# Optimization experiments

Hardware: AMD Instinct MI355X
Metric: run time of the kernel (lower is better)

Reference implementation:

```python
import jax, jax.numpy as jnp
import numpy as np

NB, HD, NL, NF = 5, 64, 4, 10           # num_bins, hidden_dim(d_model), num_layers, num_frames
DI, DS, DC, DTR = 128, 16, 4, 4          # d_inner=2*HD, d_state, d_conv, dt_rank=ceil(HD/16)
B, H, W = 4, 64, 64


def _conv2d(x, w, b):
    y = jax.lax.conv_general_dilated(x, w, (1, 1), 'SAME',
                                     dimension_numbers=('NCHW', 'OIHW', 'NCHW'))
    return y + b[None, :, None, None]


def _bn_relu(x, gamma, beta, eps=1e-5):
    # BatchNorm2d in training mode: biased batch stats over (N,H,W)
    mean = x.mean(axis=(0, 2, 3), keepdims=True)
    var = x.var(axis=(0, 2, 3), keepdims=True)
    y = (x - mean) * jax.lax.rsqrt(var + eps)
    return jax.nn.relu(y * gamma[None, :, None, None] + beta[None, :, None, None])


def _silu(x):
    return x * jax.nn.sigmoid(x)


def _causal_dwconv(x, w, b):
    # x: (B,L,DI), w: (DI,K) depthwise causal conv, b: (DI,)
    K = w.shape[1]
    L = x.shape[1]
    xp = jnp.pad(x, ((0, 0), (K - 1, 0), (0, 0)))
    y = sum(xp[:, k:k + L, :] * w[:, k] for k in range(K))
    return y + b


def _selective_scan(u, delta, A, Bm, Cm, D):
    # u,delta: (B,L,DI); A: (DI,DS); Bm,Cm: (B,L,DS); D: (DI,)
    dT, BT, CT, uT = (t.transpose(1, 0, 2) for t in (delta, Bm, Cm, u))
    h0 = jnp.zeros((u.shape[0], A.shape[0], A.shape[1]), u.dtype)

    def step(h, inp):
        d_t, B_t, C_t, u_t = inp                     # (B,DI),(B,DS),(B,DS),(B,DI)
        dA = jnp.exp(d_t[:, :, None] * A)            # (B,DI,DS)
        h = dA * h + (d_t * u_t)[:, :, None] * B_t[:, None, :]
        y = jnp.einsum('bds,bs->bd', h, C_t)
        return h, y

    _, ys = jax.lax.scan(step, h0, (dT, BT, CT, uT))  # ys: (L,B,DI)
    return ys.transpose(1, 0, 2) + u * D


def _mamba(x, in_proj, conv_w, conv_b, x_proj, dt_w, dt_b, A_log, Dp, out_proj):
    xz = x @ in_proj.T                               # (B,L,2*DI)
    xi, z = jnp.split(xz, 2, axis=-1)
    xi = _silu(_causal_dwconv(xi, conv_w, conv_b))
    xdbc = xi @ x_proj.T                             # (B,L,DTR+2*DS)
    dt, Bm, Cm = jnp.split(xdbc, [DTR, DTR + DS], axis=-1)
    delta = jax.nn.softplus(dt @ dt_w.T + dt_b)
    A = -jnp.exp(A_log)
    y = _selective_scan(xi, delta, A, Bm, Cm, Dp)
    return (y * _silu(z)) @ out_proj.T


def setup_inputs() -> dict:
    key = jax.random.key(0)
    ks = jax.random.split(key, 20)
    s = 0.02
    inp = {
        'x': jax.random.normal(ks[0], (B, NB, H, W), jnp.float32),
        'enc_w': jax.random.normal(ks[1], (HD, NB, 3, 3), jnp.float32) * s,
        'enc_b': jnp.zeros((HD,), jnp.float32),
        'enc_g': jnp.ones((HD,), jnp.float32),
        'enc_be': jnp.zeros((HD,), jnp.float32),
        'in_proj': jax.random.normal(ks[2], (NL, 2 * DI, HD), jnp.float32) * s,
        'conv_w': jax.random.normal(ks[3], (NL, DI, DC), jnp.float32) * s,
        'conv_b': jnp.zeros((NL, DI), jnp.float32),
        'x_proj': jax.random.normal(ks[4], (NL, DTR + 2 * DS, DI), jnp.float32) * s,
        'dt_w': jax.random.normal(ks[5], (NL, DI, DTR), jnp.float32) * s,
        'dt_b': jax.random.normal(ks[6], (NL, DI), jnp.float32) * 0.1 - 4.0,
        'A_log': jnp.broadcast_to(jnp.log(jnp.arange(1, DS + 1, dtype=jnp.float32)),
                                  (NL, DI, DS)).copy(),
        'Dp': jnp.ones((NL, DI), jnp.float32),
        'out_proj': jax.random.normal(ks[7], (NL, HD, DI), jnp.float32) * s,
        'dec1_w': jax.random.normal(ks[8], (HD, HD, 3, 3), jnp.float32) * s,
        'dec1_b': jnp.zeros((HD,), jnp.float32),
        'dec1_g': jnp.ones((HD,), jnp.float32),
        'dec1_be': jnp.zeros((HD,), jnp.float32),
        'dec2_w': jax.random.normal(ks[9], (NF, HD, 3, 3), jnp.float32) * s,
        'dec2_b': jnp.zeros((NF,), jnp.float32),
    }
    return inp


def reference(x, enc_w, enc_b, enc_g, enc_be, in_proj, conv_w, conv_b, x_proj,
              dt_w, dt_b, A_log, Dp, out_proj, dec1_w, dec1_b, dec1_g, dec1_be,
              dec2_w, dec2_b):
    Bb, _, Hh, Ww = x.shape
    h = _bn_relu(_conv2d(x, enc_w, enc_b), enc_g, enc_be)   # (B,HD,H,W)
    t = h.reshape(Bb, HD, Hh * Ww).transpose(0, 2, 1)        # (B,L,HD)
    for i in range(NL):
        t = t + _mamba(t, in_proj[i], conv_w[i], conv_b[i], x_proj[i],
                       dt_w[i], dt_b[i], A_log[i], Dp[i], out_proj[i])
    h = t.transpose(0, 2, 1).reshape(Bb, HD, Hh, Ww)
    h = _bn_relu(_conv2d(h, dec1_w, dec1_b), dec1_g, dec1_be)
    return _conv2d(h, dec2_w, dec2_b)                        # (B,NF,H,W)
```

## Files before the change

kernel.cpp:

```cpp
#include <hip/hip_runtime.h>
#include <hip/hip_bf16.h>

#define BB   4
#define NBC  5
#define HD   64
#define NLAYER 4
#define NFC  10
#define DIM  128
#define DSN  16
#define DCN  4
#define DTRK 4
#define HH   64
#define WWD  64
#define LL   4096
#define MM   (BB*LL)
#define NCHUNK 128
#define CLEN   32
#define TSTEP  16

__global__ void k_prep_all(const float* __restrict__ in_proj, const float* __restrict__ out_proj,
                           const float* __restrict__ dec1_w, const float* __restrict__ dec2_w,
                           float* __restrict__ wTin, float* __restrict__ wTout,
                           float* __restrict__ wT1, float* __restrict__ wT2,
                           float* __restrict__ stats, float* __restrict__ stats2) {
    int idx = blockIdx.x * blockDim.x + threadIdx.x;
    if (idx < 65536) {
        int n = idx & 255, k = (idx >> 8) & 63, l = idx >> 14;
        wTin[idx] = in_proj[(l << 14) + (n << 6) + k];
    } else if (idx < 98304) {
        int j = idx - 65536;
        int n = j & 63, k = (j >> 6) & 127, l = j >> 13;
        wTout[j] = out_proj[(l << 13) + (n << 7) + k];
    } else if (idx < 135168) {
        int j = idx - 98304;
        int co = j & 63, tap = (j >> 6) % 9, ci = j / 576;
        wT1[j] = dec1_w[co * 576 + ci * 9 + tap];
    } else if (idx < 142848) {
        int j = idx - 135168;
        int tap = j % 12, t2 = j / 12, co = t2 % NFC, ci = t2 / NFC;
        wT2[j] = (tap < 9) ? dec2_w[co * 576 + ci * 9 + tap] : 0.f;
    } else if (idx < 143104) {
        int j = idx - 142848;
        if (j < 128) stats[j] = 0.f; else stats2[j - 128] = 0.f;
    }
}

__global__ void k_enc_conv(const float* __restrict__ x, const float* __restrict__ w,
                           const float* __restrict__ bias, float* __restrict__ out,
                           float* __restrict__ stats) {
    __shared__ float r1[256], r2[256];
    int tid = threadIdx.x;
    int idx = blockIdx.x * 256 + tid;
    int wx = idx & 63;
    int hy = (idx >> 6) & 63;
    int co = (idx >> 12) & 63;
    int b  = idx >> 18;
    float acc = bias[co];
    for (int ci = 0; ci < NBC; ++ci) {
        const float* xin = x + (((long)(b * NBC + ci)) << 12);
        const float* wp  = w + (co * NBC + ci) * 9;
        #pragma unroll
        for (int kh = 0; kh < 3; ++kh) {
            int ih = hy + kh - 1;
            if (ih < 0 || ih >= HH) continue;
            #pragma unroll
            for (int kw = 0; kw < 3; ++kw) {
                int iw = wx + kw - 1;
                if (iw < 0 || iw >= WWD) continue;
                acc += xin[(ih << 6) + iw] * wp[kh * 3 + kw];
            }
        }
    }
    out[idx] = acc;
    r1[tid] = acc; r2[tid] = acc * acc;
    __syncthreads();
    for (int off = 128; off > 0; off >>= 1) {
        if (tid < off) { r1[tid] += r1[tid + off]; r2[tid] += r2[tid + off]; }
        __syncthreads();
    }
    if (tid == 0) {
        atomicAdd(&stats[co], r1[0]);
        atomicAdd(&stats[64 + co], r2[0]);
    }
}

__global__ void k_bn_tr_seq(const float* __restrict__ src, const float* __restrict__ stats,
                            const float* __restrict__ g, const float* __restrict__ be,
                            float* __restrict__ tout) {
    __shared__ float s[64 * 65];
    __shared__ float sc[64], sh[64];
    int blk = blockIdx.x;
    int b = blk >> 6;
    int hw0 = (blk & 63) << 6;
    int tid = threadIdx.x;
    if (tid < 64) {
        float m = stats[tid] * (1.f / 16384.f);
        float var = stats[64 + tid] * (1.f / 16384.f) - m * m;
        float ss = g[tid] * rsqrtf(var + 1e-5f);
        sc[tid] = ss; sh[tid] = be[tid] - m * ss;
    }
    for (int i = tid; i < 4096; i += 256) {
        int pix = i & 63, c = i >> 6;
        s[c * 65 + pix] = src[((long)((b << 6) + c) << 12) + hw0 + pix];
    }
    __syncthreads();
    for (int i = tid; i < 4096; i += 256) {
        int c = i & 63, pix = i >> 6;
        float y = s[c * 65 + pix] * sc[c] + sh[c];
        tout[((long)((b << 12) + hw0 + pix) << 6) + c] = fmaxf(y, 0.f);
    }
}

__global__ __launch_bounds__(256, 1) void k_gemm_in2(const float* __restrict__ tin,
                                                     const float* __restrict__ wT,
                                                     float* __restrict__ xz) {
    __shared__ __align__(16) float ts[64 * 68];
    long m0 = (long)blockIdx.x << 6;
    int tid = threadIdx.x;
    int rg = tid >> 5;
    int cg = tid & 31;
    for (int i = tid; i < 4096; i += 256) {
        int r = i >> 6, k = i & 63;
        ts[r * 68 + k] = tin[(m0 << 6) + i];
    }
    __syncthreads();
    float acc[8][8] = {};
    int n0 = cg << 3;
    for (int k4 = 0; k4 < 16; ++k4) {
        float4 a[8];
        #pragma unroll
        for (int r2 = 0; r2 < 8; ++r2)
            a[r2] = *(const float4*)&ts[((rg << 3) + r2) * 68 + (k4 << 2)];
        #pragma unroll
        for (int kk = 0; kk < 4; ++kk) {
            const float* wr = wT + (((k4 << 2) + kk) << 8) + n0;
            float4 w0 = *(const float4*)&wr[0];
            float4 w1 = *(const float4*)&wr[4];
            #pragma unroll
            for (int r2 = 0; r2 < 8; ++r2) {
                float av = (kk == 0) ? a[r2].x : (kk == 1) ? a[r2].y
                         : (kk == 2) ? a[r2].z : a[r2].w;
                acc[r2][0] += av * w0.x; acc[r2][1] += av * w0.y;
                acc[r2][2] += av * w0.z; acc[r2][3] += av * w0.w;
                acc[r2][4] += av * w1.x; acc[r2][5] += av * w1.y;
                acc[r2][6] += av * w1.z; acc[r2][7] += av * w1.w;
            }
        }
    }
    #pragma unroll
    for (int r2 = 0; r2 < 8; ++r2) {
        long m = m0 + (rg << 3) + r2;
        *(float4*)&xz[(m << 8) + n0]     = make_float4(acc[r2][0], acc[r2][1], acc[r2][2], acc[r2][3]);
        *(float4*)&xz[(m << 8) + n0 + 4] = make_float4(acc[r2][4], acc[r2][5], acc[r2][6], acc[r2][7]);
    }
}

__global__ __launch_bounds__(256, 1) void k_gemm_oi(const float* __restrict__ gated,
                                                    const float* __restrict__ wTo,
                                                    const float* __restrict__ wTi,
                                                    float* __restrict__ tio,
                                                    float* __restrict__ xz) {
    __shared__ __align__(16) float g_s[64 * 132];
    __shared__ __align__(16) float t_s[64 * 68];
    long m0 = (long)blockIdx.x << 6;
    int tid = threadIdx.x;
    for (int i = tid; i < 8192; i += 256) {
        int r = i >> 7, k = i & 127;
        g_s[r * 132 + k] = gated[(m0 << 7) + i];
    }
    __syncthreads();
    {
        int rg = tid >> 4, cg = tid & 15;
        int n0 = cg << 2;
        float acc[4][4] = {};
        for (int k4 = 0; k4 < 32; ++k4) {
            float4 a[4];
            #pragma unroll
            for (int r2 = 0; r2 < 4; ++r2)
                a[r2] = *(const float4*)&g_s[((rg << 2) + r2) * 132 + (k4 << 2)];
            #pragma unroll
            for (int kk = 0; kk < 4; ++kk) {
                const float* wr = wTo + (((k4 << 2) + kk) << 6) + n0;
                float4 w0 = *(const float4*)&wr[0];
                #pragma unroll
                for (int r2 = 0; r2 < 4; ++r2) {
                    float av = (kk == 0) ? a[r2].x : (kk == 1) ? a[r2].y
                             : (kk == 2) ? a[r2].z : a[r2].w;
                    acc[r2][0] += av * w0.x; acc[r2][1] += av * w0.y;
                    acc[r2][2] += av * w0.z; acc[r2][3] += av * w0.w;
                }
            }
        }
        #pragma unroll
        for (int r2 = 0; r2 < 4; ++r2) {
            long m = m0 + (rg << 2) + r2;
            float4 t0 = *(const float4*)&tio[(m << 6) + n0];
            t0.x += acc[r2][0]; t0.y += acc[r2][1];
            t0.z += acc[r2][2]; t0.w += acc[r2][3];
            *(float4*)&tio[(m << 6) + n0] = t0;
            *(float4*)&t_s[((rg << 2) + r2) * 68 + n0] = t0;
        }
    }
    __syncthreads();
    {
        int rg = tid >> 5, cg = tid & 31;
        int n0 = cg << 3;
        float acc[8][8] = {};
        for (int k4 = 0; k4 < 16; ++k4) {
            float4 a[8];
            #pragma unroll
            for (int r2 = 0; r2 < 8; ++r2)
                a[r2] = *(const float4*)&t_s[((rg << 3) + r2) * 68 + (k4 << 2)];
            #pragma unroll
            for (int kk = 0; kk < 4; ++kk) {
                const float* wr = wTi + (((k4 << 2) + kk) << 8) + n0;
                float4 w0 = *(const float4*)&wr[0];
                float4 w1 = *(const float4*)&wr[4];
                #pragma unroll
                for (int r2 = 0; r2 < 8; ++r2) {
                    float av = (kk == 0) ? a[r2].x : (kk == 1) ? a[r2].y
                             : (kk == 2) ? a[r2].z : a[r2].w;
                    acc[r2][0] += av * w0.x; acc[r2][1] += av * w0.y;
                    acc[r2][2] += av * w0.z; acc[r2][3] += av * w0.w;
                    acc[r2][4] += av * w1.x; acc[r2][5] += av * w1.y;
                    acc[r2][6] += av * w1.z; acc[r2][7] += av * w1.w;
                }
            }
        }
        #pragma unroll
        for (int r2 = 0; r2 < 8; ++r2) {
            long m = m0 + (rg << 3) + r2;
            *(float4*)&xz[(m << 8) + n0]     = make_float4(acc[r2][0], acc[r2][1], acc[r2][2], acc[r2][3]);
            *(float4*)&xz[(m << 8) + n0 + 4] = make_float4(acc[r2][4], acc[r2][5], acc[r2][6], acc[r2][7]);
        }
    }
}

__global__ __launch_bounds__(256, 1) void k_gemm_out2(const float* __restrict__ gated,
                                                      const float* __restrict__ wT,
                                                      float* __restrict__ tio) {
    __shared__ __align__(16) float ts[64 * 132];
    long m0 = (long)blockIdx.x << 6;
    int tid = threadIdx.x;
    int rg = tid >> 4;
    int cg = tid & 15;
    for (int i = tid; i < 8192; i += 256) {
        int r2 = i >> 7, k = i & 127;
        ts[r2 * 132 + k] = gated[(m0 << 7) + i];
    }
    __syncthreads();
    float acc[4][4] = {};
    int n0 = cg << 2;
    for (int k4 = 0; k4 < 32; ++k4) {
        float4 a[4];
        #pragma unroll
        for (int r2 = 0; r2 < 4; ++r2)
            a[r2] = *(const float4*)&ts[((rg << 2) + r2) * 132 + (k4 << 2)];
        #pragma unroll
        for (int kk = 0; kk < 4; ++kk) {
            const float* wr = wT + (((k4 << 2) + kk) << 6) + n0;
            float4 w0 = *(const float4*)&wr[0];
            #pragma unroll
            for (int r2 = 0; r2 < 4; ++r2) {
                float av = (kk == 0) ? a[r2].x : (kk == 1) ? a[r2].y
                         : (kk == 2) ? a[r2].z : a[r2].w;
                acc[r2][0] += av * w0.x; acc[r2][1] += av * w0.y;
                acc[r2][2] += av * w0.z; acc[r2][3] += av * w0.w;
            }
        }
    }
    #pragma unroll
    for (int r2 = 0; r2 < 4; ++r2) {
        long m = m0 + (rg << 2) + r2;
        float4 t0 = *(const float4*)&tio[(m << 6) + n0];
        t0.x += acc[r2][0]; t0.y += acc[r2][1];
        t0.z += acc[r2][2]; t0.w += acc[r2][3];
        *(float4*)&tio[(m << 6) + n0] = t0;
    }
}

__global__ void k_xproj_fused(const float* __restrict__ xz, const float* __restrict__ cw,
                              const float* __restrict__ cb, const float* __restrict__ Wx,
                              const float* __restrict__ dw, const float* __restrict__ dbias,
                              float* __restrict__ xi, float* __restrict__ xdbc,
                              float* __restrict__ delta) {
    __shared__ float xz_s[35 * 132];
    __shared__ float xi_s[32 * 132];
    __shared__ float w_s[36 * 132];
    __shared__ float xs[32 * 40];
    __shared__ float cwT[4 * 128];
    __shared__ float cb_s[128];
    long m0 = (long)blockIdx.x << 5;
    int l0 = (int)(m0 & 4095);
    int tid = threadIdx.x;

    for (int i = tid; i < 35 * 128; i += 256) {
        int j = i >> 7, k = i & 127;
        int l = l0 - 3 + j;
        float v = 0.f;
        if (l >= 0) v = xz[(m0 - 3 + j) * 256 + k];
        xz_s[j * 132 + k] = v;
    }
    if (tid < 128) cb_s[tid] = cb[tid];
    for (int i = tid; i < 512; i += 256) {
        int kk = i >> 7, di = i & 127;
        cwT[(kk << 7) + di] = cw[(di << 2) + kk];
    }
    for (int i = tid; i < 4608; i += 256) {
        int n = i >> 7, k = i & 127;
        w_s[n * 132 + k] = Wx[i];
    }
    __syncthreads();

    for (int ii = 0; ii < 4; ++ii) {
        int i = tid + (ii << 8);
        int r = i >> 5;
        int d4 = (i & 31) << 2;
        float4 a = *(const float4*)&cb_s[d4];
        #pragma unroll
        for (int kk = 0; kk < 4; ++kk) {
            float4 xv = *(const float4*)&xz_s[(r + kk) * 132 + d4];
            float4 wv = *(const float4*)&cwT[(kk << 7) + d4];
            a.x += xv.x * wv.x; a.y += xv.y * wv.y;
            a.z += xv.z * wv.z; a.w += xv.w * wv.w;
        }
        a.x = a.x / (1.f + __expf(-a.x));
        a.y = a.y / (1.f + __expf(-a.y));
        a.z = a.z / (1.f + __expf(-a.z));
        a.w = a.w / (1.f + __expf(-a.w));
        *(float4*)&xi_s[r * 132 + d4] = a;
        *(float4*)&xi[(m0 + r) * 128 + d4] = a;
    }
    __syncthreads();

    int n = tid & 63;
    int rg = tid >> 6;
    if (n < 36) {
        float acc[8] = {0,0,0,0,0,0,0,0};
        for (int k4 = 0; k4 < 32; ++k4) {
            float4 w4 = *(const float4*)&w_s[n * 132 + (k4 << 2)];
            #pragma unroll
            for (int r = 0; r < 8; ++r) {
                float4 a4 = *(const float4*)&xi_s[((rg << 3) + r) * 132 + (k4 << 2)];
                acc[r] += a4.x * w4.x + a4.y * w4.y + a4.z * w4.z + a4.w * w4.w;
            }
        }
        #pragma unroll
        for (int r = 0; r < 8; ++r) {
            int rr = (rg << 3) + r;
            xdbc[(m0 + rr) * 36 + n] = acc[r];
            xs[rr * 40 + n] = acc[r];
        }
    }
    __syncthreads();
    for (int i = tid; i < 4096; i += 256) {
        int r = i >> 7, di = i & 127;
        float v = dbias[di];
        float4 d4 = *(const float4*)&dw[di << 2];
        v += xs[r * 40 + 0] * d4.x + xs[r * 40 + 1] * d4.y
           + xs[r * 40 + 2] * d4.z + xs[r * 40 + 3] * d4.w;
        delta[(m0 + r) * 128 + di] = (v > 20.f) ? v : log1pf(expf(v));
    }
}

__global__ void k_scan_p1(const float* __restrict__ delta, const float* __restrict__ xi,
                          const float* __restrict__ xdbc, const float* __restrict__ A_log,
                          float* __restrict__ Pb, float* __restrict__ Sb) {
    __shared__ float d_s[TSTEP][64];
    __shared__ float u_s[TSTEP][64];
    __shared__ float b_s[TSTEP][16];
    int chunk = blockIdx.x, b = blockIdx.y, half = blockIdx.z;
    int tid = threadIdx.x;
    int dq = tid & 3;
    int dil = tid >> 2;
    int di = (half << 6) + dil;
    float4 al = *(const float4*)&A_log[(di << 4) + (dq << 2)];
    float Av[4] = { -expf(al.x), -expf(al.y), -expf(al.z), -expf(al.w) };
    float h[4] = {0.f, 0.f, 0.f, 0.f};
    float P[4] = {1.f, 1.f, 1.f, 1.f};
    long t0 = ((long)b << 12) + (long)chunk * CLEN;

    int srow = tid >> 4, sc4 = (tid & 15) << 2;
    for (int tile = 0; tile < CLEN / TSTEP; ++tile) {
        __syncthreads();
        long ls = t0 + tile * TSTEP + srow;
        *(float4*)&d_s[srow][sc4] = *(const float4*)&delta[(ls << 7) + (half << 6) + sc4];
        *(float4*)&u_s[srow][sc4] = *(const float4*)&xi[(ls << 7) + (half << 6) + sc4];
        if (tid < 64) {
            int r2 = tid >> 2, cc = (tid & 3) << 2;
            long l2 = t0 + tile * TSTEP + r2;
            *(float4*)&b_s[r2][cc] = *(const float4*)&xdbc[l2 * 36 + DTRK + cc];
        }
        __syncthreads();
        #pragma unroll
        for (int i = 0; i < TSTEP; ++i) {
            float d = d_s[i][dil];
            float u = u_s[i][dil];
            float du = d * u;
            float4 Bv = *(float4*)&b_s[i][dq << 2];
            float a0 = __expf(d * Av[0]); h[0] = a0 * h[0] + du * Bv.x; P[0] *= a0;
            float a1 = __expf(d * Av[1]); h[1] = a1 * h[1] + du * Bv.y; P[1] *= a1;
            float a2 = __expf(d * Av[2]); h[2] = a2 * h[2] + du * Bv.z; P[2] *= a2;
            float a3 = __expf(d * Av[3]); h[3] = a3 * h[3] + du * Bv.w; P[3] *= a3;
        }
    }
    long o = (((long)chunk * BB + b) << 11) + (di << 4) + (dq << 2);
    *(float4*)&Pb[o] = make_float4(P[0], P[1], P[2], P[3]);
    *(float4*)&Sb[o] = make_float4(h[0], h[1], h[2], h[3]);
}

__global__ void k_scan_p2(float* Pb, const float* __restrict__ Sb) {
    int t = blockIdx.x * blockDim.x + threadIdx.x;
    int b = t >> 11;
    int s = t & 2047;
    float h = 0.f;
    for (int c = 0; c < NCHUNK; ++c) {
        long idx = (((long)c * BB + b) << 11) + s;
        float p = Pb[idx];
        float sv = Sb[idx];
        Pb[idx] = h;
        h = p * h + sv;
    }
}

__global__ void k_scan_p3(const float* __restrict__ delta, const float* __restrict__ xi,
                          const float* __restrict__ xdbc, const float* __restrict__ A_log,
                          const float* __restrict__ Dp, const float* __restrict__ xz,
                          const float* __restrict__ hin, float* __restrict__ gated) {
    __shared__ float d_s[TSTEP][64];
    __shared__ float u_s[TSTEP][64];
    __shared__ float bc_s[TSTEP][32];
    __shared__ float y_s[TSTEP][64];
    int chunk = blockIdx.x, b = blockIdx.y, half = blockIdx.z;
    int tid = threadIdx.x;
    int dq = tid & 3;
    int dil = tid >> 2;
    int di = (half << 6) + dil;
    float4 al = *(const float4*)&A_log[(di << 4) + (dq << 2)];
    float Av[4] = { -expf(al.x), -expf(al.y), -expf(al.z), -expf(al.w) };
    float Dv = Dp[di];
    long ho = (((long)chunk * BB + b) << 11) + (di << 4) + (dq << 2);
    float4 h4 = *(const float4*)&hin[ho];
    float h[4] = { h4.x, h4.y, h4.z, h4.w };
    long t0 = ((long)b << 12) + (long)chunk * CLEN;

    int srow = tid >> 4, sc4 = (tid & 15) << 2;
    for (int tile = 0; tile < CLEN / TSTEP; ++tile) {
        __syncthreads();
        long ls = t0 + tile * TSTEP + srow;
        *(float4*)&d_s[srow][sc4] = *(const float4*)&delta[(ls << 7) + (half << 6) + sc4];
        *(float4*)&u_s[srow][sc4] = *(const float4*)&xi[(ls << 7) + (half << 6) + sc4];
        if (tid < 128) {
            int r2 = tid >> 3, cc = (tid & 7) << 2;
            long l2 = t0 + tile * TSTEP + r2;
            *(float4*)&bc_s[r2][cc] = *(const float4*)&xdbc[l2 * 36 + DTRK + cc];
        }
        __syncthreads();
        #pragma unroll
        for (int i = 0; i < TSTEP; ++i) {
            float d = d_s[i][dil];
            float u = u_s[i][dil];
            float du = d * u;
            float4 Bv = *(float4*)&bc_s[i][dq << 2];
            float4 Cv = *(float4*)&bc_s[i][16 + (dq << 2)];
            float a0 = __expf(d * Av[0]); h[0] = a0 * h[0] + du * Bv.x;
            float a1 = __expf(d * Av[1]); h[1] = a1 * h[1] + du * Bv.y;
            float a2 = __expf(d * Av[2]); h[2] = a2 * h[2] + du * Bv.z;
            float a3 = __expf(d * Av[3]); h[3] = a3 * h[3] + du * Bv.w;
            float yp = h[0] * Cv.x + h[1] * Cv.y + h[2] * Cv.z + h[3] * Cv.w;
            yp += __shfl_xor(yp, 1);
            yp += __shfl_xor(yp, 2);
            if (dq == 0)
                y_s[i][dil] = yp + u * Dv;
        }
        __syncthreads();
        {
            long l = t0 + tile * TSTEP + srow;
            float4 y4 = *(float4*)&y_s[srow][sc4];
            float4 z4 = *(const float4*)&xz[(l << 8) + DIM + (half << 6) + sc4];
            float4 og;
            og.x = y4.x * (z4.x / (1.f + __expf(-z4.x)));
            og.y = y4.y * (z4.y / (1.f + __expf(-z4.y)));
            og.z = y4.z * (z4.z / (1.f + __expf(-z4.z)));
            og.w = y4.w * (z4.w / (1.f + __expf(-z4.w)));
            *(float4*)&gated[(l << 7) + (half << 6) + sc4] = og;
        }
    }
}

__global__ __launch_bounds__(256, 1) void k_dec1_new(const float* __restrict__ tin,
                                                     const float* __restrict__ wT,
                                                     const float* __restrict__ bias,
                                                     float* __restrict__ out,
                                                     float* __restrict__ stats2) {
    __shared__ __align__(16) float x_s[64 * 132];
    __shared__ __align__(16) float w_s[4 * 4608];
    int tile = blockIdx.x;
    int b = blockIdx.y;
    int ty0 = (tile >> 3) << 3;
    int tx0 = (tile & 7) << 3;
    int tid = threadIdx.x;
    int wv = tid >> 6;
    int lane = tid & 63;
    int r = lane >> 3;
    int cg = lane & 7;

    for (int i = tid; i < 6400; i += 256) {
        int pl = i >> 6;
        int c = i & 63;
        int py = pl / 10, px = pl - py * 10;
        int ih = ty0 + py - 1, iw = tx0 + px - 1;
        float v = 0.f;
        if (ih >= 0 && ih < HH && iw >= 0 && iw < WWD)
            v = tin[(((long)((b << 12) + (ih << 6) + iw)) << 6) + c];
        x_s[c * 132 + py * 12 + px] = v;
    }
    float* myw = &w_s[wv * 4608];
    const float* gw = wT + (wv * 16) * 576;
    float4 pref[18];
    #pragma unroll
    for (int i = 0; i < 18; ++i)
        pref[i] = *(const float4*)&gw[(i * 64 + lane) * 4];
    #pragma unroll
    for (int i = 0; i < 18; ++i)
        *(float4*)&myw[(i * 64 + lane) * 4] = pref[i];
    __syncthreads();

    float acc[8][8] = {};
    #pragma unroll
    for (int ch = 0; ch < 2; ++ch) {
        if (ch == 0) {
            const float* gw1 = wT + (wv * 16 + 8) * 576;
            #pragma unroll
            for (int i = 0; i < 18; ++i)
                pref[i] = *(const float4*)&gw1[(i * 64 + lane) * 4];
        }
        for (int cl = 0; cl < 8; ++cl) {
            int cib = wv * 16 + ch * 8 + cl;
            float xrow[3][10];
            #pragma unroll
            for (int kh = 0; kh < 3; ++kh) {
                const float* xr = &x_s[cib * 132 + (r + kh) * 12];
                float4 a0 = *(const float4*)&xr[0];
                float4 a1 = *(const float4*)&xr[4];
                float2 a2 = *(const float2*)&xr[8];
                xrow[kh][0] = a0.x; xrow[kh][1] = a0.y; xrow[kh][2] = a0.z; xrow[kh][3] = a0.w;
                xrow[kh][4] = a1.x; xrow[kh][5] = a1.y; xrow[kh][6] = a1.z; xrow[kh][7] = a1.w;
                xrow[kh][8] = a2.x; xrow[kh][9] = a2.y;
            }
            const float* wp = &myw[cl * 576];
            #pragma unroll
            for (int kh = 0; kh < 3; ++kh) {
                #pragma unroll
                for (int kw = 0; kw < 3; ++kw) {
                    const float* wp2 = wp + (kh * 3 + kw) * 64 + (cg << 3);
                    float4 wa = *(const float4*)&wp2[0];
                    float4 wb = *(const float4*)&wp2[4];
                    #pragma unroll
                    for (int j = 0; j < 8; ++j) {
                        float xv = xrow[kh][kw + j];
                        acc[j][0] += xv * wa.x; acc[j][1] += xv * wa.y;
                        acc[j][2] += xv * wa.z; acc[j][3] += xv * wa.w;
                        acc[j][4] += xv * wb.x; acc[j][5] += xv * wb.y;
                        acc[j][6] += xv * wb.z; acc[j][7] += xv * wb.w;
                    }
                }
            }
        }
        if (ch == 0) {
            #pragma unroll
            for (int i = 0; i < 18; ++i)
                *(float4*)&myw[(i * 64 + lane) * 4] = pref[i];
        }
    }

    #pragma unroll
    for (int j = 0; j < 8; ++j) {
        *(float4*)&myw[lane * 68 + (j << 3)]     = make_float4(acc[j][0], acc[j][1], acc[j][2], acc[j][3]);
        *(float4*)&myw[lane * 68 + (j << 3) + 4] = make_float4(acc[j][4], acc[j][5], acc[j][6], acc[j][7]);
    }
    __syncthreads();

    float bv = bias[lane];
    float ssum = 0.f, ssq = 0.f;
    #pragma unroll
    for (int pp = 0; pp < 16; ++pp) {
        int pr = (wv << 1) + (pp >> 3);
        int pc = pp & 7;
        int ol = (pr << 3) + (lane >> 3);
        int ix = (pc << 3) + (lane & 7);
        float s = w_s[ol * 68 + ix] + w_s[4608 + ol * 68 + ix]
                + w_s[9216 + ol * 68 + ix] + w_s[13824 + ol * 68 + ix] + bv;
        out[(((long)((b << 12) + ((ty0 + pr) << 6) + tx0 + pc)) << 6) + lane] = s;
        ssum += s; ssq += s * s;
    }
    float* red = x_s;
    red[(wv << 6) + lane] = ssum;
    red[256 + (wv << 6) + lane] = ssq;
    __syncthreads();
    if (tid < 64) {
        float a = red[tid] + red[64 + tid] + red[128 + tid] + red[192 + tid];
        float q = red[256 + tid] + red[320 + tid] + red[384 + tid] + red[448 + tid];
        atomicAdd(&stats2[tid], a);
        atomicAdd(&stats2[64 + tid], q);
    }
}

__global__ void k_dec2_fused(const float* __restrict__ src, const float* __restrict__ stats2,
                             const float* __restrict__ g, const float* __restrict__ be,
                             const float* __restrict__ wT, const float* __restrict__ bias,
                             float* __restrict__ out) {
    __shared__ float x_s[64 * 101];
    __shared__ float w_s[64 * NFC * 12];
    __shared__ float sc_s[64];
    __shared__ float sh_s[64];
    int tile = blockIdx.x;
    int b = blockIdx.y;
    int ty0 = (tile >> 3) << 3;
    int tx0 = (tile & 7) << 3;
    int tid = threadIdx.x;

    if (tid < 64) {
        float m = stats2[tid] * (1.f / 16384.f);
        float var = stats2[64 + tid] * (1.f / 16384.f) - m * m;
        float s = g[tid] * rsqrtf(var + 1e-5f);
        sc_s[tid] = s;
        sh_s[tid] = be[tid] - m * s;
    }
    for (int i = tid; i < 64 * NFC * 12; i += 256)
        w_s[i] = wT[i];
    __syncthreads();

    for (int i = tid; i < 6400; i += 256) {
        int pl = i >> 6;
        int c = i & 63;
        int py = pl / 10, px = pl - py * 10;
        int ih = ty0 + py - 1, iw = tx0 + px - 1;
        float v = 0.f;
        if (ih >= 0 && ih < HH && iw >= 0 && iw < WWD) {
            v = src[((long)((b << 12) + (ih << 6) + iw)) * 64 + c];
            v = fmaxf(v * sc_s[c] + sh_s[c], 0.f);
        }
        x_s[c * 101 + pl] = v;
    }
    __syncthreads();

    int px = tid & 63;
    int py = px >> 3, pxx = px & 7;
    int cog = tid >> 6;
    float acc[3] = {0.f, 0.f, 0.f};
    int nco = (cog < 2) ? 3 : 2;

    for (int ci = 0; ci < 64; ++ci) {
        const float* xr = &x_s[ci * 101 + py * 10 + pxx];
        float xv[9];
        #pragma unroll
        for (int kh = 0; kh < 3; ++kh)
            #pragma unroll
            for (int kw = 0; kw < 3; ++kw)
                xv[kh * 3 + kw] = xr[kh * 10 + kw];
        #pragma unroll
        for (int j = 0; j < 3; ++j) {
            if (j >= nco) break;
            int co = cog + (j << 2);
            const float* wp = &w_s[(ci * NFC + co) * 12];
            float4 w0 = *(const float4*)&wp[0];
            float4 w1 = *(const float4*)&wp[4];
            float  w8 = wp[8];
            acc[j] += xv[0] * w0.x + xv[1] * w0.y + xv[2] * w0.z + xv[3] * w0.w
                    + xv[4] * w1.x + xv[5] * w1.y + xv[6] * w1.z + xv[7] * w1.w
                    + xv[8] * w8;
        }
    }
    int hw = ((ty0 + py) << 6) + tx0 + pxx;
    #pragma unroll
    for (int j = 0; j < 3; ++j) {
        if (j >= nco) break;
        int co = cog + (j << 2);
        out[((long)(b * NFC + co) << 12) + hw] = acc[j] + bias[co];
    }
}

extern "C" void kernel_launch(void* const* d_in, const int* in_sizes, int n_in,
                              void* d_out, int out_size, void* d_ws, size_t ws_size,
                              hipStream_t stream) {
    const float* x       = (const float*)d_in[0];
    const float* enc_w   = (const float*)d_in[1];
    const float* enc_b   = (const float*)d_in[2];
    const float* enc_g   = (const float*)d_in[3];
    const float* enc_be  = (const float*)d_in[4];
    const float* in_proj = (const float*)d_in[5];
    const float* conv_w  = (const float*)d_in[6];
    const float* conv_b  = (const float*)d_in[7];
    const float* x_proj  = (const float*)d_in[8];
    const float* dt_w    = (const float*)d_in[9];
    const float* dt_b    = (const float*)d_in[10];
    const float* A_log   = (const float*)d_in[11];
    const float* Dp      = (const float*)d_in[12];
    const float* out_prj = (const float*)d_in[13];
    const float* dec1_w  = (const float*)d_in[14];
    const float* dec1_b  = (const float*)d_in[15];
    const float* dec1_g  = (const float*)d_in[16];
    const float* dec1_be = (const float*)d_in[17];
    const float* dec2_w  = (const float*)d_in[18];
    const float* dec2_b  = (const float*)d_in[19];
    float* out = (float*)d_out;

    float* ws = (float*)d_ws;
    size_t off = 0;
    float* conv_buf  = ws + off; off += 1048576;
    float* stats     = ws + off; off += 128;
    float* stats2    = ws + off; off += 128;
    float* wT1       = ws + off; off += 36864;
    float* wT2       = ws + off; off += 7680;
    float* wTin      = ws + off; off += 65536;
    float* wTout     = ws + off; off += 32768;
    float* t_buf     = ws + off; off += 1048576;
    float* xz_buf    = ws + off; off += 4194304;
    float* xi_buf    = ws + off; off += 2097152;
    float* xdbc_buf  = ws + off; off += 589824;
    float* delta_buf = ws + off; off += 2097152;
    float* gated_buf = ws + off; off += 2097152;
    (void)ws_size; (void)in_sizes; (void)n_in; (void)out_size;

    float* Pb = conv_buf;
    float* Sb = gated_buf;

    k_prep_all<<<560, 256, 0, stream>>>(in_proj, out_prj, dec1_w, dec2_w,
                                        wTin, wTout, wT1, wT2, stats, stats2);

    k_enc_conv<<<4096, 256, 0, stream>>>(x, enc_w, enc_b, conv_buf, stats);
    k_bn_tr_seq<<<256, 256, 0, stream>>>(conv_buf, stats, enc_g, enc_be, t_buf);

    dim3 sg(NCHUNK, BB, 2);
    k_gemm_in2<<<256, 256, 0, stream>>>(t_buf, wTin, xz_buf);
    for (int i = 0; i < NLAYER; ++i) {
        k_xproj_fused<<<512, 256, 0, stream>>>(xz_buf, conv_w + i * DIM * DCN,
                                               conv_b + i * DIM, x_proj + i * 36 * DIM,
                                               dt_w + i * DIM * DTRK, dt_b + i * DIM,
                                               xi_buf, xdbc_buf, delta_buf);
        k_scan_p1<<<sg, 256, 0, stream>>>(delta_buf, xi_buf, xdbc_buf,
                                          A_log + i * DIM * DSN, Pb, Sb);
        k_scan_p2<<<32, 256, 0, stream>>>(Pb, Sb);
        k_scan_p3<<<sg, 256, 0, stream>>>(delta_buf, xi_buf, xdbc_buf,
                                          A_log + i * DIM * DSN, Dp + i * DIM,
                                          xz_buf, Pb, gated_buf);
        if (i < NLAYER - 1)
            k_gemm_oi<<<256, 256, 0, stream>>>(gated_buf, wTout + i * 8192,
                                               wTin + (i + 1) * 16384, t_buf, xz_buf);
    }
    k_gemm_out2<<<256, 256, 0, stream>>>(gated_buf, wTout + 3 * 8192, t_buf);

    dim3 dg1(64, BB);
    k_dec1_new<<<dg1, 256, 0, stream>>>(t_buf, wT1, dec1_b, conv_buf, stats2);
    k_dec2_fused<<<dg1, 256, 0, stream>>>(conv_buf, stats2, dec1_g, dec1_be, wT2, dec2_b, out);
}
```

Before: 532.4 us.

## Fuse chunked scan pass 1 into xproj kernel using shared-memory delta and B

The first chunk-scan pass (per-chunk decay product and local state) now runs at the end of the xproj kernel. It uses delta, xi and B values that are already in shared memory, so the separate k_scan_p1 launch and its global re-reads of delta, xi and xdbc go away. Each thread now handles 8 states for one channel, and a launch bound of 256 threads with 2 blocks is added. The risks are higher register pressure and fewer blocks doing the sequential 32-step loop, which could lengthen this kernel's tail.

```diff
diff --git a/kernel.cpp b/kernel.cpp
--- a/kernel.cpp
+++ b/kernel.cpp
@@ -279,11 +279,13 @@
     }
 }
 
-__global__ void k_xproj_fused(const float* __restrict__ xz, const float* __restrict__ cw,
-                              const float* __restrict__ cb, const float* __restrict__ Wx,
-                              const float* __restrict__ dw, const float* __restrict__ dbias,
-                              float* __restrict__ xi, float* __restrict__ xdbc,
-                              float* __restrict__ delta) {
+__global__ __launch_bounds__(256, 2) void k_xproj_fused(
+        const float* __restrict__ xz, const float* __restrict__ cw,
+        const float* __restrict__ cb, const float* __restrict__ Wx,
+        const float* __restrict__ dw, const float* __restrict__ dbias,
+        const float* __restrict__ A_log,
+        float* __restrict__ xi, float* __restrict__ xdbc,
+        float* __restrict__ delta, float* __restrict__ Pb, float* __restrict__ Sb) {
     __shared__ float xz_s[35 * 132];
     __shared__ float xi_s[32 * 132];
     __shared__ float w_s[36 * 132];
@@ -292,6 +294,8 @@
     __shared__ float cb_s[128];
     long m0 = (long)blockIdx.x << 5;
     int l0 = (int)(m0 & 4095);
+    int b = (int)(m0 >> 12);
+    int chunk = l0 >> 5;
     int tid = threadIdx.x;
 
     for (int i = tid; i < 35 * 128; i += 256) {
@@ -353,60 +357,51 @@
         }
     }
     __syncthreads();
+
+    float* delta_s = xz_s;
     for (int i = tid; i < 4096; i += 256) {
         int r = i >> 7, di = i & 127;
         float v = dbias[di];
         float4 d4 = *(const float4*)&dw[di << 2];
         v += xs[r * 40 + 0] * d4.x + xs[r * 40 + 1] * d4.y
            + xs[r * 40 + 2] * d4.z + xs[r * 40 + 3] * d4.w;
-        delta[(m0 + r) * 128 + di] = (v > 20.f) ? v : log1pf(expf(v));
-    }
-}
-
-__global__ void k_scan_p1(const float* __restrict__ delta, const float* __restrict__ xi,
-                          const float* __restrict__ xdbc, const float* __restrict__ A_log,
-                          float* __restrict__ Pb, float* __restrict__ Sb) {
-    __shared__ float d_s[TSTEP][64];
-    __shared__ float u_s[TSTEP][64];
-    __shared__ float b_s[TSTEP][16];
-    int chunk = blockIdx.x, b = blockIdx.y, half = blockIdx.z;
-    int tid = threadIdx.x;
-    int dq = tid & 3;
-    int dil = tid >> 2;
-    int di = (half << 6) + dil;
-    float4 al = *(const float4*)&A_log[(di << 4) + (dq << 2)];
-    float Av[4] = { -expf(al.x), -expf(al.y), -expf(al.z), -expf(al.w) };
-    float h[4] = {0.f, 0.f, 0.f, 0.f};
-    float P[4] = {1.f, 1.f, 1.f, 1.f};
-    long t0 = ((long)b << 12) + (long)chunk * CLEN;
-
-    int srow = tid >> 4, sc4 = (tid & 15) << 2;
-    for (int tile = 0; tile < CLEN / TSTEP; ++tile) {
-        __syncthreads();
-        long ls = t0 + tile * TSTEP + srow;
-        *(float4*)&d_s[srow][sc4] = *(const float4*)&delta[(ls << 7) + (half << 6) + sc4];
-        *(float4*)&u_s[srow][sc4] = *(const float4*)&xi[(ls << 7) + (half << 6) + sc4];
-        if (tid < 64) {
-            int r2 = tid >> 2, cc = (tid & 3) << 2;
-            long l2 = t0 + tile * TSTEP + r2;
-            *(float4*)&b_s[r2][cc] = *(const float4*)&xdbc[l2 * 36 + DTRK + cc];
-        }
-        __syncthreads();
-        #pragma unroll
-        for (int i = 0; i < TSTEP; ++i) {
-            float d = d_s[i][dil];
-            float u = u_s[i][dil];
+        float sp = (v > 20.f) ? v : log1pf(expf(v));
+        delta[(m0 + r) * 128 + di] = sp;
+        delta_s[r * 132 + di] = sp;
+    }
+    __syncthreads();
+
+    {
+        int di = tid >> 1;
+        int dso = (tid & 1) << 3;
+        float4 al0 = *(const float4*)&A_log[(di << 4) + dso];
+        float4 al1 = *(const float4*)&A_log[(di << 4) + dso + 4];
+        float Av[8] = { -expf(al0.x), -expf(al0.y), -expf(al0.z), -expf(al0.w),
+                        -expf(al1.x), -expf(al1.y), -expf(al1.z), -expf(al1.w) };
+        float h[8] = {0,0,0,0,0,0,0,0};
+        float P[8] = {1,1,1,1,1,1,1,1};
+        #pragma unroll 4
+        for (int i = 0; i < CLEN; ++i) {
+            float d = delta_s[i * 132 + di];
+            float u = xi_s[i * 132 + di];
             float du = d * u;
-            float4 Bv = *(float4*)&b_s[i][dq << 2];
-            float a0 = __expf(d * Av[0]); h[0] = a0 * h[0] + du * Bv.x; P[0] *= a0;
-            float a1 = __expf(d * Av[1]); h[1] = a1 * h[1] + du * Bv.y; P[1] *= a1;
-            float a2 = __expf(d * Av[2]); h[2] = a2 * h[2] + du * Bv.z; P[2] *= a2;
-            float a3 = __expf(d * Av[3]); h[3] = a3 * h[3] + du * Bv.w; P[3] *= a3;
-        }
-    }
-    long o = (((long)chunk * BB + b) << 11) + (di << 4) + (dq << 2);
-    *(float4*)&Pb[o] = make_float4(P[0], P[1], P[2], P[3]);
-    *(float4*)&Sb[o] = make_float4(h[0], h[1], h[2], h[3]);
+            float4 B0 = *(float4*)&xs[i * 40 + DTRK + dso];
+            float4 B1 = *(float4*)&xs[i * 40 + DTRK + dso + 4];
+            float a0 = __expf(d * Av[0]); h[0] = a0 * h[0] + du * B0.x; P[0] *= a0;
+            float a1 = __expf(d * Av[1]); h[1] = a1 * h[1] + du * B0.y; P[1] *= a1;
+            float a2 = __expf(d * Av[2]); h[2] = a2 * h[2] + du * B0.z; P[2] *= a2;
+            float a3 = __expf(d * Av[3]); h[3] = a3 * h[3] + du * B0.w; P[3] *= a3;
+            float a4 = __expf(d * Av[4]); h[4] = a4 * h[4] + du * B1.x; P[4] *= a4;
+            float a5 = __expf(d * Av[5]); h[5] = a5 * h[5] + du * B1.y; P[5] *= a5;
+            float a6 = __expf(d * Av[6]); h[6] = a6 * h[6] + du * B1.z; P[6] *= a6;
+            float a7 = __expf(d * Av[7]); h[7] = a7 * h[7] + du * B1.w; P[7] *= a7;
+        }
+        long o = (((long)chunk * BB + b) << 11) + (di << 4) + dso;
+        *(float4*)&Pb[o]     = make_float4(P[0], P[1], P[2], P[3]);
+        *(float4*)&Pb[o + 4] = make_float4(P[4], P[5], P[6], P[7]);
+        *(float4*)&Sb[o]     = make_float4(h[0], h[1], h[2], h[3]);
+        *(float4*)&Sb[o + 4] = make_float4(h[4], h[5], h[6], h[7]);
+    }
 }
 
 __global__ void k_scan_p2(float* Pb, const float* __restrict__ Sb) {
@@ -738,9 +733,8 @@
         k_xproj_fused<<<512, 256, 0, stream>>>(xz_buf, conv_w + i * DIM * DCN,
                                                conv_b + i * DIM, x_proj + i * 36 * DIM,
                                                dt_w + i * DIM * DTRK, dt_b + i * DIM,
-                                               xi_buf, xdbc_buf, delta_buf);
-        k_scan_p1<<<sg, 256, 0, stream>>>(delta_buf, xi_buf, xdbc_buf,
-                                          A_log + i * DIM * DSN, Pb, Sb);
+                                               A_log + i * DIM * DSN,
+                                               xi_buf, xdbc_buf, delta_buf, Pb, Sb);
         k_scan_p2<<<32, 256, 0, stream>>>(Pb, Sb);
         k_scan_p3<<<sg, 256, 0, stream>>>(delta_buf, xi_buf, xdbc_buf,
                                           A_log + i * DIM * DSN, Dp + i * DIM,
```

Result: faster. 511.2 us (-4.0%).
